# Kernel tuning notes

Measured on AMD Instinct MI355X. Metric: run time of the kernel, lower is better.

Reference implementation:

```python
import jax, jax.numpy as jnp
import numpy as np

B, N, D = 4, 4096, 512
E, H, TOPK = 4, 2048, 1
V_MAX, FEAT_CLAMP = 3.0, 10.0


def setup_inputs() -> dict:
    key = jax.random.key(0)
    ks = jax.random.split(key, 8)
    g = lambda k, shape, s: (jax.random.normal(k, shape, jnp.float32) * s)
    return {
        "x": g(ks[0], (B, N, D), 1.0),
        "gate_w": g(ks[1], (D, E), 0.02), "gate_b": jnp.zeros((E,), jnp.float32),
        "w1": g(ks[2], (E, D, H), 0.02), "b1": jnp.zeros((E, H), jnp.float32),
        "w2": g(ks[3], (E, H, D), 0.02), "b2": jnp.zeros((E, D), jnp.float32),
        "v_w": g(ks[4], (D,), 0.02), "v_b": jnp.zeros((), jnp.float32),
        "out_w": g(ks[5], (2, D), 0.02), "out_b": jnp.zeros((D,), jnp.float32),
        "bk_scale": jnp.asarray(1.0, jnp.float32),
    }


def _moe_ffn(x, gate_w, gate_b, w1, b1, w2, b2):
    # Sparse MoE FFN (eval mode, no dropout): top-k routing, softmax over top-k logits.
    logits = x @ gate_w + gate_b                       # (B,N,E)
    vals, idx = jax.lax.top_k(logits, TOPK)            # (B,N,K)
    wts = jax.nn.softmax(vals, axis=-1)                # (B,N,K); == 1.0 for top_k=1
    wfull = jnp.sum(jax.nn.one_hot(idx, E, dtype=x.dtype) * wts[..., None], axis=-2)  # (B,N,E)
    h = jax.nn.gelu(jnp.einsum('bnd,edh->benh', x, w1) + b1[None, :, None, :])
    y = jnp.einsum('benh,ehd->bend', h, w2) + b2[None, :, None, :]
    return jnp.einsum('bne,bend->bnd', wfull, y)


def _tridiag_green_diag(diag, sup, sub, z):
    # Diagonal of G = (T - z I)^{-1} for tridiagonal T via stable continuant ratios:
    #   L_i = theta_i/theta_{i-1},  R_i = phi_i/phi_{i+1},  G_ii = 1/(L_i + R_i - d_i)
    d = diag.astype(jnp.complex64) - z                 # (B,N)
    s = (sub * sup).astype(jnp.complex64)              # (B,N-1)
    dT = jnp.swapaxes(d, 0, 1)                         # (N,B)
    sT = jnp.swapaxes(s, 0, 1)                         # (N-1,B)

    def step(carry, inp):
        di, si = inp
        nxt = di - si / carry
        return nxt, nxt

    _, Lrest = jax.lax.scan(step, dT[0], (dT[1:], sT))
    L = jnp.concatenate([dT[:1], Lrest], axis=0)       # (N,B)
    _, Rrest = jax.lax.scan(step, dT[-1], (dT[:-1][::-1], sT[::-1]))
    R = jnp.concatenate([dT[-1:], Rrest], axis=0)[::-1]
    G = 1.0 / (L + R - dT)                             # (N,B)
    return jnp.swapaxes(G, 0, 1)                       # (B,N)


def reference(x, gate_w, gate_b, w1, b1, w2, b2, v_w, v_b, out_w, out_b, bk_scale):
    ffn_out = _moe_ffn(x, gate_w, gate_b, w1, b1, w2, b2)        # (B,N,D)
    v = jnp.clip(ffn_out @ v_w + v_b, -V_MAX, V_MAX)             # (B,N)
    he_diag = v - 2.0                                            # h0_diag_base = -2
    ones_off = jnp.ones((x.shape[0], x.shape[1] - 1), x.dtype)   # h0 sub/super = 1
    G = _tridiag_green_diag(he_diag, ones_off, ones_off, jnp.complex64(1j))
    feats = jnp.clip(jnp.stack([G.real, G.imag], axis=-1), -FEAT_CLAMP, FEAT_CLAMP)  # (B,N,2)
    spec = feats @ out_w + out_b                                 # (B,N,D)
    return ffn_out + bk_scale * spec
```

## Files before the change

### kernel.cpp

```cpp
#include <hip/hip_runtime.h>
#include <hip/hip_bf16.h>
#include <stdint.h>

#define TOK 16384
#define NSEQ 4096
#define BATCH 4
#define Dm 512
#define Em 4
#define Hm 2048

typedef __attribute__((ext_vector_type(4))) float f32x4;
typedef __attribute__((ext_vector_type(4))) unsigned int u32x4;

__device__ __forceinline__ unsigned short f2bf(float f) {
    union { float f; uint32_t u; } v; v.f = f;
    uint32_t u = v.u;
    uint32_t r = (u + 0x7FFFu + ((u >> 16) & 1u)) >> 16;
    return (unsigned short)r;
}

struct cpx { float re, im; };
__device__ __forceinline__ cpx cmul(cpx a, cpx b) { return { a.re*b.re - a.im*b.im, a.re*b.im + a.im*b.re }; }
__device__ __forceinline__ cpx csub(cpx a, cpx b) { return { a.re - b.re, a.im - b.im }; }
__device__ __forceinline__ cpx cadd(cpx a, cpx b) { return { a.re + b.re, a.im + b.im }; }
__device__ __forceinline__ cpx cdiv(cpx a, cpx b) {
    float inv = 1.0f / (b.re*b.re + b.im*b.im);
    return { (a.re*b.re + a.im*b.im)*inv, (a.im*b.re - a.re*b.im)*inv };
}

__device__ __forceinline__ void mfma_bf16(f32x4& acc, u32x4 a, u32x4 b) {
    asm("v_mfma_f32_16x16x32_bf16 %0, %1, %2, %0" : "+v"(acc) : "v"(a), "v"(b));
}

#define GLOAD_LDS16(g, l) \
    __builtin_amdgcn_global_load_lds((const __attribute__((address_space(1))) unsigned int*)(g), \
                                     (__attribute__((address_space(3))) unsigned int*)(l), 16, 0, 0)

__global__ __launch_bounds__(256) void gate_kernel(
    const float* __restrict__ x, const float* __restrict__ gate_w, const float* __restrict__ gate_b,
    unsigned short* __restrict__ xbf, int* __restrict__ expert_id)
{
    int wid = threadIdx.x >> 6, lane = threadIdx.x & 63;
    int t0 = (blockIdx.x * 4 + wid) * 8;

    const float4* gw4 = (const float4*)gate_w;
    float4 g[8];
#pragma unroll
    for (int j = 0; j < 8; j++) g[j] = gw4[lane * 8 + j];
    double gb0 = (double)gate_b[0], gb1 = (double)gate_b[1];
    double gb2 = (double)gate_b[2], gb3 = (double)gate_b[3];

    for (int tt = 0; tt < 8; tt++) {
        int t = t0 + tt;
        const float4* x4 = (const float4*)(x + (size_t)t * Dm);
        float4 xa = x4[lane * 2], xb = x4[lane * 2 + 1];

        uint4 pk;
        pk.x = (uint32_t)f2bf(xa.x) | ((uint32_t)f2bf(xa.y) << 16);
        pk.y = (uint32_t)f2bf(xa.z) | ((uint32_t)f2bf(xa.w) << 16);
        pk.z = (uint32_t)f2bf(xb.x) | ((uint32_t)f2bf(xb.y) << 16);
        pk.w = (uint32_t)f2bf(xb.z) | ((uint32_t)f2bf(xb.w) << 16);
        *(uint4*)(xbf + (size_t)t * Dm + lane * 8) = pk;

        float xv[8] = { xa.x, xa.y, xa.z, xa.w, xb.x, xb.y, xb.z, xb.w };
        double s0 = 0, s1 = 0, s2 = 0, s3 = 0;
#pragma unroll
        for (int j = 0; j < 8; j++) {
            s0 += (double)xv[j] * (double)g[j].x;
            s1 += (double)xv[j] * (double)g[j].y;
            s2 += (double)xv[j] * (double)g[j].z;
            s3 += (double)xv[j] * (double)g[j].w;
        }
#pragma unroll
        for (int off = 1; off < 64; off <<= 1) {
            s0 += __shfl_xor(s0, off);
            s1 += __shfl_xor(s1, off);
            s2 += __shfl_xor(s2, off);
            s3 += __shfl_xor(s3, off);
        }
        if (lane == 0) {
            double l0 = s0 + gb0, l1 = s1 + gb1, l2 = s2 + gb2, l3 = s3 + gb3;
            int e = 0; double best = l0;
            if (l1 > best) { best = l1; e = 1; }
            if (l2 > best) { best = l2; e = 2; }
            if (l3 > best) { best = l3; e = 3; }
            expert_id[t] = e;
        }
    }
}

__global__ __launch_bounds__(256) void transpose_cvt(
    const float* __restrict__ w1, const float* __restrict__ w2,
    unsigned short* __restrict__ w1t, unsigned short* __restrict__ w2t)
{
    int z = blockIdx.z;
    const float* src; unsigned short* dst; int R, C;
    if (z < 4) { src = w1 + (size_t)z * Dm * Hm; dst = w1t + (size_t)z * Hm * Dm; R = Dm; C = Hm; }
    else       { src = w2 + (size_t)(z - 4) * Hm * Dm; dst = w2t + (size_t)(z - 4) * Dm * Hm; R = Hm; C = Dm; }
    int c0 = blockIdx.x * 32, r0 = blockIdx.y * 32;
    if (c0 >= C || r0 >= R) return;
    __shared__ float tile[32][33];
    int tx = threadIdx.x & 31, ty = threadIdx.x >> 5;
#pragma unroll
    for (int i = 0; i < 4; i++)
        tile[ty + i * 8][tx] = src[(size_t)(r0 + ty + i * 8) * C + c0 + tx];
    __syncthreads();
#pragma unroll
    for (int i = 0; i < 4; i++)
        dst[(size_t)(c0 + ty + i * 8) * R + r0 + tx] = f2bf(tile[tx][ty + i * 8]);
}

__global__ __launch_bounds__(1024) void route_kernel(
    const int* __restrict__ expert_id, int* __restrict__ counts,
    int* __restrict__ offsets, int* __restrict__ rowmap)
{
    __shared__ int wcnt[16][4];
    __shared__ int woff[16][4];
    int wid = threadIdx.x >> 6, lane = threadIdx.x & 63;
    int base = wid * 1024;

    int myeid[16], myrank[16];
    int run0 = 0, run1 = 0, run2 = 0, run3 = 0;
#pragma unroll
    for (int s = 0; s < 16; s++) {
        int e = expert_id[base + s * 64 + lane];
        myeid[s] = e;
        unsigned long long b0 = __ballot(e & 1);
        unsigned long long b1 = __ballot(e & 2);
        unsigned long long m0 = (e & 1) ? b0 : ~b0;
        unsigned long long m1 = (e & 2) ? b1 : ~b1;
        unsigned long long same = m0 & m1;
        unsigned long long below = same & ((1ull << lane) - 1ull);
        int runh = (e == 0) ? run0 : (e == 1) ? run1 : (e == 2) ? run2 : run3;
        myrank[s] = runh + (int)__popcll(below);
        run0 += (int)__popcll(~b0 & ~b1);
        run1 += (int)__popcll(b0 & ~b1);
        run2 += (int)__popcll(~b0 & b1);
        run3 += (int)__popcll(b0 & b1);
    }
    if (lane == 0) {
        wcnt[wid][0] = run0; wcnt[wid][1] = run1; wcnt[wid][2] = run2; wcnt[wid][3] = run3;
    }
    __syncthreads();
    if (threadIdx.x == 0) {
        int t0 = 0, t1 = 0, t2 = 0, t3 = 0;
        for (int w = 0; w < 16; w++) {
            woff[w][0] = t0; woff[w][1] = t1; woff[w][2] = t2; woff[w][3] = t3;
            t0 += wcnt[w][0]; t1 += wcnt[w][1]; t2 += wcnt[w][2]; t3 += wcnt[w][3];
        }
        counts[0] = t0; counts[1] = t1; counts[2] = t2; counts[3] = t3;
        int o0 = 0, o1 = t0, o2 = t0 + t1, o3 = t0 + t1 + t2;
        offsets[0] = o0; offsets[1] = o1; offsets[2] = o2; offsets[3] = o3;
        for (int w = 0; w < 16; w++) {
            woff[w][0] += o0; woff[w][1] += o1; woff[w][2] += o2; woff[w][3] += o3;
        }
    }
    __syncthreads();
#pragma unroll
    for (int s = 0; s < 16; s++) {
        int e = myeid[s];
        rowmap[woff[wid][e] + myrank[s]] = base + s * 64 + lane;
    }
}

template<int KTOT, int NTOT, bool GATHER_A, bool GELU_EPI>
__global__ __launch_bounds__(256) void gemm_kernel(
    const unsigned short* __restrict__ A, const unsigned short* __restrict__ B,
    const float* __restrict__ bias,
    const int* __restrict__ counts, const int* __restrict__ offsets,
    const int* __restrict__ rowmap,
    unsigned short* __restrict__ Hout, float* __restrict__ Cout,
    const float* __restrict__ v_w, float* __restrict__ vpart)
{
    constexpr int NT = KTOT / 32;
    int e = blockIdx.z;
    int Me = counts[e];
    int mblk = blockIdx.x;
    if (mblk * 128 >= Me) return;
    int base = offsets[e];
    int nblk = blockIdx.y;
    int t = threadIdx.x, wid = t >> 6, lane = t & 63;

    __shared__ __align__(16) unsigned short As[3][128 * 32];
    __shared__ __align__(16) unsigned short Bs[3][128 * 32];

    const unsigned short* agp[2];
    const unsigned short* bgp[2];
#pragma unroll
    for (int c = 0; c < 2; c++) {
        int r = (c * 4 + wid) * 16 + (lane >> 2);
        int g = (lane & 3) ^ ((r >> 1) & 3);
        int mr = mblk * 128 + r; if (mr >= Me) mr = Me - 1;
        int arow = GATHER_A ? rowmap[base + mr] : (base + mr);
        agp[c] = A + (size_t)arow * KTOT + g * 8;
        int nr = nblk * 128 + r;
        bgp[c] = B + ((size_t)e * NTOT + nr) * (size_t)KTOT + g * 8;
    }

    int wm = wid >> 1, wn = wid & 1;
    int g = lane >> 4;
    int r0a = wm * 64 + (lane & 15);
    int r0b = wn * 64 + (lane & 15);
    int abase = r0a * 64 + ((g ^ ((r0a >> 1) & 3)) << 4);
    int bbase = r0b * 64 + ((g ^ ((r0b >> 1) & 3)) << 4);

    f32x4 acc[4][4] = {};

#define STAGE_T(bufi, kt) do { \
    _Pragma("unroll") \
    for (int c = 0; c < 2; c++) { \
        GLOAD_LDS16(agp[c] + (kt) * 32, &As[bufi][(c * 4 + wid) * 512]); \
        GLOAD_LDS16(bgp[c] + (kt) * 32, &Bs[bufi][(c * 4 + wid) * 512]); \
    } \
} while (0)

    STAGE_T(0, 0);
    STAGE_T(1, 1);
    int cur = 0;
    for (int kt = 0; kt < NT; ++kt) {
        int nb = cur + 2; if (nb >= 3) nb -= 3;
        if (kt + 2 < NT) {
            STAGE_T(nb, kt + 2);
            asm volatile("s_waitcnt vmcnt(8)" ::: "memory");
        } else if (kt + 1 < NT) {
            asm volatile("s_waitcnt vmcnt(4)" ::: "memory");
        } else {
            asm volatile("s_waitcnt vmcnt(0)" ::: "memory");
        }
        __builtin_amdgcn_s_barrier();

        const char* ab = (const char*)&As[cur][0];
        const char* bb = (const char*)&Bs[cur][0];
        u32x4 av[4], bv[4];
#pragma unroll
        for (int m = 0; m < 4; m++) av[m] = *(const u32x4*)(ab + abase + m * 1024);
#pragma unroll
        for (int n = 0; n < 4; n++) bv[n] = *(const u32x4*)(bb + bbase + n * 1024);
        __builtin_amdgcn_s_setprio(1);
#pragma unroll
        for (int m = 0; m < 4; m++)
#pragma unroll
            for (int n = 0; n < 4; n++)
                mfma_bf16(acc[m][n], av[m], bv[n]);
        __builtin_amdgcn_s_setprio(0);
        asm volatile("s_waitcnt lgkmcnt(0)" ::: "memory");
        __builtin_amdgcn_s_barrier();
        cur = (cur + 1 == 3) ? 0 : cur + 1;
    }
#undef STAGE_T

    float bb4[4], vw4[4];
#pragma unroll
    for (int n = 0; n < 4; n++) {
        int col = nblk * 128 + wn * 64 + n * 16 + (lane & 15);
        bb4[n] = bias[e * NTOT + col];
        if (!GELU_EPI) vw4[n] = v_w[col];
    }
#pragma unroll
    for (int m = 0; m < 4; m++) {
        int rbase = wm * 64 + m * 16 + ((lane >> 4) << 2);
#pragma unroll
        for (int j = 0; j < 4; j++) {
            int row = mblk * 128 + rbase + j;
            bool ok = row < Me;
            float p = 0.0f;
            int tok = 0;
            if (!GELU_EPI) tok = rowmap[base + (ok ? row : 0)];
#pragma unroll
            for (int n = 0; n < 4; n++) {
                int col = nblk * 128 + wn * 64 + n * 16 + (lane & 15);
                float v = acc[m][n][j] + bb4[n];
                if (GELU_EPI) {
                    if (ok) {
                        float u = 0.7978845608f * (v + 0.044715f * v * v * v);
                        float ex = __expf(2.0f * u);
                        float th = 1.0f - 2.0f / (ex + 1.0f);
                        float hv = 0.5f * v * (1.0f + th);
                        Hout[(size_t)(base + row) * NTOT + col] = f2bf(hv);
                    }
                } else {
                    if (ok) Cout[(size_t)tok * Dm + col] = v;
                    p += v * vw4[n];
                }
            }
            if (!GELU_EPI) {
                p += __shfl_xor(p, 1); p += __shfl_xor(p, 2);
                p += __shfl_xor(p, 4); p += __shfl_xor(p, 8);
                if (ok && (lane & 15) == 0) vpart[tok * 4 + nblk] = p;
            }
        }
    }
}

__global__ __launch_bounds__(256) void vdot2_kernel(
    const float4* __restrict__ vpart, const float* __restrict__ v_b, float* __restrict__ dre)
{
    int t = blockIdx.x * 256 + threadIdx.x;
    float4 p = vpart[t];
    float v = p.x + p.y + p.z + p.w + v_b[0];
    v = fminf(fmaxf(v, -3.0f), 3.0f);
    dre[t] = v - 2.0f;
}

#define SDI(i) ((i) + ((i) >> 6))
__global__ __launch_bounds__(64) void scan_kernel(
    const float* __restrict__ dre, float2* __restrict__ Lf, float2* __restrict__ Rb)
{
    int b = blockIdx.x >> 1, dir = blockIdx.x & 1;
    int lane = threadIdx.x;
    __shared__ float sd[4096 + 64];
    const float* src = dre + b * NSEQ;
    for (int i = lane; i < NSEQ; i += 64)
        sd[SDI(i)] = src[dir ? (NSEQ - 1 - i) : i];
    __syncthreads();

    cpx m00 = {1, 0}, m01 = {0, 0}, m10 = {0, 0}, m11 = {1, 0};
    int s0i = lane * 64;
#pragma unroll 4
    for (int j = 0; j < 64; j++) {
        cpx d = { sd[SDI(s0i + j)], -1.0f };
        cpx n00 = csub(cmul(d, m00), m10);
        cpx n01 = csub(cmul(d, m01), m11);
        m10 = m00; m11 = m01; m00 = n00; m01 = n01;
        if ((j & 15) == 15) {
            float mx = fmaxf(fmaxf(fmaxf(fabsf(m00.re), fabsf(m00.im)), fmaxf(fabsf(m01.re), fabsf(m01.im))),
                             fmaxf(fmaxf(fabsf(m10.re), fabsf(m10.im)), fmaxf(fabsf(m11.re), fabsf(m11.im))));
            float r = 1.0f / mx;
            m00.re *= r; m00.im *= r; m01.re *= r; m01.im *= r;
            m10.re *= r; m10.im *= r; m11.re *= r; m11.im *= r;
        }
    }

#pragma unroll
    for (int off = 1; off < 64; off <<= 1) {
        cpx q00, q01, q10, q11;
        q00.re = __shfl_up(m00.re, off); q00.im = __shfl_up(m00.im, off);
        q01.re = __shfl_up(m01.re, off); q01.im = __shfl_up(m01.im, off);
        q10.re = __shfl_up(m10.re, off); q10.im = __shfl_up(m10.im, off);
        q11.re = __shfl_up(m11.re, off); q11.im = __shfl_up(m11.im, off);
        if (lane >= off) {
            cpx r00 = cadd(cmul(m00, q00), cmul(m01, q10));
            cpx r01 = cadd(cmul(m00, q01), cmul(m01, q11));
            cpx r10 = cadd(cmul(m10, q00), cmul(m11, q10));
            cpx r11 = cadd(cmul(m10, q01), cmul(m11, q11));
            m00 = r00; m01 = r01; m10 = r10; m11 = r11;
            float mx = fmaxf(fmaxf(fmaxf(fabsf(m00.re), fabsf(m00.im)), fmaxf(fabsf(m01.re), fabsf(m01.im))),
                             fmaxf(fmaxf(fabsf(m10.re), fabsf(m10.im)), fmaxf(fabsf(m11.re), fabsf(m11.im))));
            float r = 1.0f / mx;
            m00.re *= r; m00.im *= r; m01.re *= r; m01.im *= r;
            m10.re *= r; m10.im *= r; m11.re *= r; m11.im *= r;
        }
    }

    cpx e00, e10;
    e00.re = __shfl_up(m00.re, 1); e00.im = __shfl_up(m00.im, 1);
    e10.re = __shfl_up(m10.re, 1); e10.im = __shfl_up(m10.im, 1);
    if (lane == 0) { e00 = {1, 0}; e10 = {0, 0}; }

    float2* outp = dir ? Rb : Lf;
    cpx Linv = cdiv(e10, e00);
#pragma unroll 4
    for (int j = 0; j < 64; j++) {
        int p = s0i + j;
        cpx d = { sd[SDI(p)], -1.0f };
        cpx L = csub(d, Linv);
        int idx = dir ? (NSEQ - 1 - p) : p;
        outp[b * NSEQ + idx] = make_float2(L.re, L.im);
        float inv = 1.0f / (L.re * L.re + L.im * L.im);
        Linv.re = L.re * inv; Linv.im = -L.im * inv;
    }
}

__global__ __launch_bounds__(256) void final_kernel(
    float* __restrict__ out, const float* __restrict__ dre,
    const float2* __restrict__ Lf, const float2* __restrict__ Rb,
    const float* __restrict__ out_w, const float* __restrict__ out_b,
    const float* __restrict__ bk)
{
    int t = blockIdx.x * 2 + (threadIdx.x >> 7);
    int c = threadIdx.x & 127;
    float2 L = Lf[t], R = Rb[t];
    float dr = dre[t];
    float denr = L.x + R.x - dr;
    float deni = L.y + R.y + 1.0f;
    float inv = 1.0f / (denr * denr + deni * deni);
    float f0 = fminf(fmaxf(denr * inv, -10.0f), 10.0f);
    float f1 = fminf(fmaxf(-deni * inv, -10.0f), 10.0f);
    float bks = bk[0];
    const float4* ow0 = (const float4*)out_w;
    const float4* ow1 = (const float4*)(out_w + Dm);
    const float4* ob4 = (const float4*)out_b;
    float4* o4 = (float4*)(out + (size_t)t * Dm);
    float4 w0 = ow0[c], w1v = ow1[c], ob = ob4[c];
    float4 y = o4[c];
    y.x += bks * (f0 * w0.x + f1 * w1v.x + ob.x);
    y.y += bks * (f0 * w0.y + f1 * w1v.y + ob.y);
    y.z += bks * (f0 * w0.z + f1 * w1v.z + ob.z);
    y.w += bks * (f0 * w0.w + f1 * w1v.w + ob.w);
    o4[c] = y;
}

constexpr size_t OFF_XBF    = 0;
constexpr size_t OFF_W1T    = 16777216;
constexpr size_t OFF_W2T    = OFF_W1T + 8388608;
constexpr size_t OFF_H      = OFF_W2T + 8388608;
constexpr size_t OFF_ROWMAP = OFF_H + 67108864;
constexpr size_t OFF_EID    = OFF_ROWMAP + 65536;
constexpr size_t OFF_DRE    = OFF_EID + 65536;
constexpr size_t OFF_LF     = OFF_DRE + 65536;
constexpr size_t OFF_RB     = OFF_LF + 131072;
constexpr size_t OFF_CNT    = OFF_RB + 131072;
constexpr size_t OFF_VPART  = OFF_CNT + 64;

extern "C" void kernel_launch(void* const* d_in, const int* in_sizes, int n_in,
                              void* d_out, int out_size, void* d_ws, size_t ws_size,
                              hipStream_t stream)
{
    const float* x      = (const float*)d_in[0];
    const float* gate_w = (const float*)d_in[1];
    const float* gate_b = (const float*)d_in[2];
    const float* w1     = (const float*)d_in[3];
    const float* b1     = (const float*)d_in[4];
    const float* w2     = (const float*)d_in[5];
    const float* b2     = (const float*)d_in[6];
    const float* v_w    = (const float*)d_in[7];
    const float* v_b    = (const float*)d_in[8];
    const float* out_w  = (const float*)d_in[9];
    const float* out_b  = (const float*)d_in[10];
    const float* bk     = (const float*)d_in[11];
    float* out = (float*)d_out;
    char* ws = (char*)d_ws;

    unsigned short* xbf = (unsigned short*)(ws + OFF_XBF);
    unsigned short* w1t = (unsigned short*)(ws + OFF_W1T);
    unsigned short* w2t = (unsigned short*)(ws + OFF_W2T);
    unsigned short* hbf = (unsigned short*)(ws + OFF_H);
    int* rowmap  = (int*)(ws + OFF_ROWMAP);
    int* eid     = (int*)(ws + OFF_EID);
    float* dre   = (float*)(ws + OFF_DRE);
    float2* Lf   = (float2*)(ws + OFF_LF);
    float2* Rb   = (float2*)(ws + OFF_RB);
    int* counts  = (int*)(ws + OFF_CNT);
    int* offsets = counts + 4;
    float* vpart = (float*)(ws + OFF_VPART);

    (void)in_sizes; (void)n_in; (void)out_size; (void)ws_size;

    gate_kernel<<<TOK / 32, 256, 0, stream>>>(x, gate_w, gate_b, xbf, eid);
    transpose_cvt<<<dim3(64, 64, 8), 256, 0, stream>>>(w1, w2, w1t, w2t);
    route_kernel<<<1, 1024, 0, stream>>>(eid, counts, offsets, rowmap);

    gemm_kernel<512, 2048, true, true><<<dim3(128, 16, 4), 256, 0, stream>>>(
        xbf, w1t, b1, counts, offsets, rowmap, hbf, nullptr, nullptr, nullptr);
    gemm_kernel<2048, 512, false, false><<<dim3(128, 4, 4), 256, 0, stream>>>(
        hbf, w2t, b2, counts, offsets, rowmap, nullptr, out, v_w, vpart);

    vdot2_kernel<<<TOK / 256, 256, 0, stream>>>((const float4*)vpart, v_b, dre);
    scan_kernel<<<8, 64, 0, stream>>>(dre, Lf, Rb);
    final_kernel<<<TOK / 2, 256, 0, stream>>>(out, dre, Lf, Rb, out_w, out_b, bk);
}
```

Measured before the change: 198.9 us.

## Merge prep kernels, narrow GEMM2 N-tile, and reorder GEMM1 block grid

Merges the gate/bf16-cast kernel and the weight transpose kernel into one launch using a flat block index. The second GEMM now uses a 64-wide N tile, doubling its block count for better CU occupancy, and vpart/vdot2 are widened to 8 partials per token to match. GEMM1 swaps its grid so that N-blocks vary fastest, which keeps A tiles reused across neighbouring blocks. It also adds launch_bounds minimum occupancy of 4, which could cause register pressure or spills.

```diff
diff --git a/kernel.cpp b/kernel.cpp
--- a/kernel.cpp
+++ b/kernel.cpp
@@ -36,69 +36,80 @@
     __builtin_amdgcn_global_load_lds((const __attribute__((address_space(1))) unsigned int*)(g), \
                                      (__attribute__((address_space(3))) unsigned int*)(l), 16, 0, 0)
 
-__global__ __launch_bounds__(256) void gate_kernel(
+#define GATE_BLOCKS 512
+#define W1T_BLOCKS 4096
+#define W2T_BLOCKS 4096
+__global__ __launch_bounds__(256) void prep_kernel(
     const float* __restrict__ x, const float* __restrict__ gate_w, const float* __restrict__ gate_b,
-    unsigned short* __restrict__ xbf, int* __restrict__ expert_id)
-{
-    int wid = threadIdx.x >> 6, lane = threadIdx.x & 63;
-    int t0 = (blockIdx.x * 4 + wid) * 8;
-
-    const float4* gw4 = (const float4*)gate_w;
-    float4 g[8];
-#pragma unroll
-    for (int j = 0; j < 8; j++) g[j] = gw4[lane * 8 + j];
-    double gb0 = (double)gate_b[0], gb1 = (double)gate_b[1];
-    double gb2 = (double)gate_b[2], gb3 = (double)gate_b[3];
-
-    for (int tt = 0; tt < 8; tt++) {
-        int t = t0 + tt;
-        const float4* x4 = (const float4*)(x + (size_t)t * Dm);
-        float4 xa = x4[lane * 2], xb = x4[lane * 2 + 1];
-
-        uint4 pk;
-        pk.x = (uint32_t)f2bf(xa.x) | ((uint32_t)f2bf(xa.y) << 16);
-        pk.y = (uint32_t)f2bf(xa.z) | ((uint32_t)f2bf(xa.w) << 16);
-        pk.z = (uint32_t)f2bf(xb.x) | ((uint32_t)f2bf(xb.y) << 16);
-        pk.w = (uint32_t)f2bf(xb.z) | ((uint32_t)f2bf(xb.w) << 16);
-        *(uint4*)(xbf + (size_t)t * Dm + lane * 8) = pk;
-
-        float xv[8] = { xa.x, xa.y, xa.z, xa.w, xb.x, xb.y, xb.z, xb.w };
-        double s0 = 0, s1 = 0, s2 = 0, s3 = 0;
-#pragma unroll
-        for (int j = 0; j < 8; j++) {
-            s0 += (double)xv[j] * (double)g[j].x;
-            s1 += (double)xv[j] * (double)g[j].y;
-            s2 += (double)xv[j] * (double)g[j].z;
-            s3 += (double)xv[j] * (double)g[j].w;
-        }
-#pragma unroll
-        for (int off = 1; off < 64; off <<= 1) {
-            s0 += __shfl_xor(s0, off);
-            s1 += __shfl_xor(s1, off);
-            s2 += __shfl_xor(s2, off);
-            s3 += __shfl_xor(s3, off);
-        }
-        if (lane == 0) {
-            double l0 = s0 + gb0, l1 = s1 + gb1, l2 = s2 + gb2, l3 = s3 + gb3;
-            int e = 0; double best = l0;
-            if (l1 > best) { best = l1; e = 1; }
-            if (l2 > best) { best = l2; e = 2; }
-            if (l3 > best) { best = l3; e = 3; }
-            expert_id[t] = e;
-        }
-    }
-}
-
-__global__ __launch_bounds__(256) void transpose_cvt(
     const float* __restrict__ w1, const float* __restrict__ w2,
+    unsigned short* __restrict__ xbf, int* __restrict__ expert_id,
     unsigned short* __restrict__ w1t, unsigned short* __restrict__ w2t)
 {
-    int z = blockIdx.z;
-    const float* src; unsigned short* dst; int R, C;
-    if (z < 4) { src = w1 + (size_t)z * Dm * Hm; dst = w1t + (size_t)z * Hm * Dm; R = Dm; C = Hm; }
-    else       { src = w2 + (size_t)(z - 4) * Hm * Dm; dst = w2t + (size_t)(z - 4) * Dm * Hm; R = Hm; C = Dm; }
-    int c0 = blockIdx.x * 32, r0 = blockIdx.y * 32;
-    if (c0 >= C || r0 >= R) return;
+    int bid = blockIdx.x;
+    if (bid < GATE_BLOCKS) {
+        int wid = threadIdx.x >> 6, lane = threadIdx.x & 63;
+        int t0 = (bid * 4 + wid) * 8;
+        const float4* gw4 = (const float4*)gate_w;
+        float4 g[8];
+#pragma unroll
+        for (int j = 0; j < 8; j++) g[j] = gw4[lane * 8 + j];
+        double gb0 = (double)gate_b[0], gb1 = (double)gate_b[1];
+        double gb2 = (double)gate_b[2], gb3 = (double)gate_b[3];
+
+        for (int tt = 0; tt < 8; tt++) {
+            int t = t0 + tt;
+            const float4* x4 = (const float4*)(x + (size_t)t * Dm);
+            float4 xa = x4[lane * 2], xb = x4[lane * 2 + 1];
+
+            uint4 pk;
+            pk.x = (uint32_t)f2bf(xa.x) | ((uint32_t)f2bf(xa.y) << 16);
+            pk.y = (uint32_t)f2bf(xa.z) | ((uint32_t)f2bf(xa.w) << 16);
+            pk.z = (uint32_t)f2bf(xb.x) | ((uint32_t)f2bf(xb.y) << 16);
+            pk.w = (uint32_t)f2bf(xb.z) | ((uint32_t)f2bf(xb.w) << 16);
+            *(uint4*)(xbf + (size_t)t * Dm + lane * 8) = pk;
+
+            float xv[8] = { xa.x, xa.y, xa.z, xa.w, xb.x, xb.y, xb.z, xb.w };
+            double s0 = 0, s1 = 0, s2 = 0, s3 = 0;
+#pragma unroll
+            for (int j = 0; j < 8; j++) {
+                s0 += (double)xv[j] * (double)g[j].x;
+                s1 += (double)xv[j] * (double)g[j].y;
+                s2 += (double)xv[j] * (double)g[j].z;
+                s3 += (double)xv[j] * (double)g[j].w;
+            }
+#pragma unroll
+            for (int off = 1; off < 64; off <<= 1) {
+                s0 += __shfl_xor(s0, off);
+                s1 += __shfl_xor(s1, off);
+                s2 += __shfl_xor(s2, off);
+                s3 += __shfl_xor(s3, off);
+            }
+            if (lane == 0) {
+                double l0 = s0 + gb0, l1 = s1 + gb1, l2 = s2 + gb2, l3 = s3 + gb3;
+                int e = 0; double best = l0;
+                if (l1 > best) { best = l1; e = 1; }
+                if (l2 > best) { best = l2; e = 2; }
+                if (l3 > best) { best = l3; e = 3; }
+                expert_id[t] = e;
+            }
+        }
+        return;
+    }
+
+    const float* src; unsigned short* dst; int R, C, c0, r0;
+    if (bid < GATE_BLOCKS + W1T_BLOCKS) {
+        int idx = bid - GATE_BLOCKS;
+        int e = idx >> 10, rem = idx & 1023;
+        src = w1 + (size_t)e * Dm * Hm; dst = w1t + (size_t)e * Hm * Dm;
+        R = Dm; C = Hm;
+        c0 = (rem >> 4) * 32; r0 = (rem & 15) * 32;
+    } else {
+        int idx = bid - GATE_BLOCKS - W1T_BLOCKS;
+        int e = idx >> 10, rem = idx & 1023;
+        src = w2 + (size_t)e * Hm * Dm; dst = w2t + (size_t)e * Dm * Hm;
+        R = Hm; C = Dm;
+        c0 = (rem >> 6) * 32; r0 = (rem & 63) * 32;
+    }
     __shared__ float tile[32][33];
     int tx = threadIdx.x & 31, ty = threadIdx.x >> 5;
 #pragma unroll
@@ -163,8 +174,8 @@
     }
 }
 
-template<int KTOT, int NTOT, bool GATHER_A, bool GELU_EPI>
-__global__ __launch_bounds__(256) void gemm_kernel(
+template<int KTOT, int NTOT, int BN, bool MSWAP, bool GATHER_A, bool GELU_EPI>
+__global__ __launch_bounds__(256, 4) void gemm_kernel(
     const unsigned short* __restrict__ A, const unsigned short* __restrict__ B,
     const float* __restrict__ bias,
     const int* __restrict__ counts, const int* __restrict__ offsets,
@@ -173,45 +184,54 @@
     const float* __restrict__ v_w, float* __restrict__ vpart)
 {
     constexpr int NT = KTOT / 32;
+    constexpr int NREP = BN / 32;
+    constexpr int BLOADS = BN / 64;
     int e = blockIdx.z;
     int Me = counts[e];
-    int mblk = blockIdx.x;
+    int mblk = MSWAP ? blockIdx.x : blockIdx.y;
     if (mblk * 128 >= Me) return;
     int base = offsets[e];
-    int nblk = blockIdx.y;
+    int nblk = MSWAP ? blockIdx.y : blockIdx.x;
     int t = threadIdx.x, wid = t >> 6, lane = t & 63;
 
     __shared__ __align__(16) unsigned short As[3][128 * 32];
-    __shared__ __align__(16) unsigned short Bs[3][128 * 32];
+    __shared__ __align__(16) unsigned short Bs[3][BN * 32];
 
     const unsigned short* agp[2];
-    const unsigned short* bgp[2];
 #pragma unroll
     for (int c = 0; c < 2; c++) {
-        int r = (c * 4 + wid) * 16 + (lane >> 2);
-        int g = (lane & 3) ^ ((r >> 1) & 3);
+        int f = c * 256 + t;
+        int r = f >> 2;
+        int g = (f & 3) ^ ((r >> 1) & 3);
         int mr = mblk * 128 + r; if (mr >= Me) mr = Me - 1;
         int arow = GATHER_A ? rowmap[base + mr] : (base + mr);
         agp[c] = A + (size_t)arow * KTOT + g * 8;
-        int nr = nblk * 128 + r;
+    }
+    const unsigned short* bgp[BLOADS];
+#pragma unroll
+    for (int c = 0; c < BLOADS; c++) {
+        int f = c * 256 + t;
+        int r = f >> 2;
+        int g = (f & 3) ^ ((r >> 1) & 3);
+        int nr = nblk * BN + r;
         bgp[c] = B + ((size_t)e * NTOT + nr) * (size_t)KTOT + g * 8;
     }
 
     int wm = wid >> 1, wn = wid & 1;
     int g = lane >> 4;
     int r0a = wm * 64 + (lane & 15);
-    int r0b = wn * 64 + (lane & 15);
+    int r0b = wn * (BN / 2) + (lane & 15);
     int abase = r0a * 64 + ((g ^ ((r0a >> 1) & 3)) << 4);
     int bbase = r0b * 64 + ((g ^ ((r0b >> 1) & 3)) << 4);
 
-    f32x4 acc[4][4] = {};
+    f32x4 acc[4][NREP] = {};
 
 #define STAGE_T(bufi, kt) do { \
+    GLOAD_LDS16(agp[0] + (kt) * 32, &As[bufi][(size_t)(0 * 4 + wid) * 512]); \
+    GLOAD_LDS16(agp[1] + (kt) * 32, &As[bufi][(size_t)(1 * 4 + wid) * 512]); \
     _Pragma("unroll") \
-    for (int c = 0; c < 2; c++) { \
-        GLOAD_LDS16(agp[c] + (kt) * 32, &As[bufi][(c * 4 + wid) * 512]); \
-        GLOAD_LDS16(bgp[c] + (kt) * 32, &Bs[bufi][(c * 4 + wid) * 512]); \
-    } \
+    for (int c = 0; c < BLOADS; c++) \
+        GLOAD_LDS16(bgp[c] + (kt) * 32, &Bs[bufi][(size_t)(c * 4 + wid) * 512]); \
 } while (0)
 
     STAGE_T(0, 0);
@@ -221,9 +241,11 @@
         int nb = cur + 2; if (nb >= 3) nb -= 3;
         if (kt + 2 < NT) {
             STAGE_T(nb, kt + 2);
-            asm volatile("s_waitcnt vmcnt(8)" ::: "memory");
+            if constexpr (BN == 128) asm volatile("s_waitcnt vmcnt(8)" ::: "memory");
+            else                     asm volatile("s_waitcnt vmcnt(6)" ::: "memory");
         } else if (kt + 1 < NT) {
-            asm volatile("s_waitcnt vmcnt(4)" ::: "memory");
+            if constexpr (BN == 128) asm volatile("s_waitcnt vmcnt(4)" ::: "memory");
+            else                     asm volatile("s_waitcnt vmcnt(3)" ::: "memory");
         } else {
             asm volatile("s_waitcnt vmcnt(0)" ::: "memory");
         }
@@ -231,16 +253,16 @@
 
         const char* ab = (const char*)&As[cur][0];
         const char* bb = (const char*)&Bs[cur][0];
-        u32x4 av[4], bv[4];
+        u32x4 av[4], bv[NREP];
 #pragma unroll
         for (int m = 0; m < 4; m++) av[m] = *(const u32x4*)(ab + abase + m * 1024);
 #pragma unroll
-        for (int n = 0; n < 4; n++) bv[n] = *(const u32x4*)(bb + bbase + n * 1024);
+        for (int n = 0; n < NREP; n++) bv[n] = *(const u32x4*)(bb + bbase + n * 1024);
         __builtin_amdgcn_s_setprio(1);
 #pragma unroll
         for (int m = 0; m < 4; m++)
 #pragma unroll
-            for (int n = 0; n < 4; n++)
+            for (int n = 0; n < NREP; n++)
                 mfma_bf16(acc[m][n], av[m], bv[n]);
         __builtin_amdgcn_s_setprio(0);
         asm volatile("s_waitcnt lgkmcnt(0)" ::: "memory");
@@ -249,10 +271,10 @@
     }
 #undef STAGE_T
 
-    float bb4[4], vw4[4];
-#pragma unroll
-    for (int n = 0; n < 4; n++) {
-        int col = nblk * 128 + wn * 64 + n * 16 + (lane & 15);
+    float bb4[NREP], vw4[NREP];
+#pragma unroll
+    for (int n = 0; n < NREP; n++) {
+        int col = nblk * BN + wn * (BN / 2) + n * 16 + (lane & 15);
         bb4[n] = bias[e * NTOT + col];
         if (!GELU_EPI) vw4[n] = v_w[col];
     }
@@ -267,8 +289,8 @@
             int tok = 0;
             if (!GELU_EPI) tok = rowmap[base + (ok ? row : 0)];
 #pragma unroll
-            for (int n = 0; n < 4; n++) {
-                int col = nblk * 128 + wn * 64 + n * 16 + (lane & 15);
+            for (int n = 0; n < NREP; n++) {
+                int col = nblk * BN + wn * (BN / 2) + n * 16 + (lane & 15);
                 float v = acc[m][n][j] + bb4[n];
                 if (GELU_EPI) {
                     if (ok) {
@@ -286,7 +308,7 @@
             if (!GELU_EPI) {
                 p += __shfl_xor(p, 1); p += __shfl_xor(p, 2);
                 p += __shfl_xor(p, 4); p += __shfl_xor(p, 8);
-                if (ok && (lane & 15) == 0) vpart[tok * 4 + nblk] = p;
+                if (ok && (lane & 15) == 0) vpart[(size_t)tok * (NTOT / BN) + nblk] = p;
             }
         }
     }
@@ -296,8 +318,8 @@
     const float4* __restrict__ vpart, const float* __restrict__ v_b, float* __restrict__ dre)
 {
     int t = blockIdx.x * 256 + threadIdx.x;
-    float4 p = vpart[t];
-    float v = p.x + p.y + p.z + p.w + v_b[0];
+    float4 a = vpart[t * 2], b = vpart[t * 2 + 1];
+    float v = a.x + a.y + a.z + a.w + b.x + b.y + b.z + b.w + v_b[0];
     v = fminf(fmaxf(v, -3.0f), 3.0f);
     dre[t] = v - 2.0f;
 }
@@ -446,13 +468,13 @@
 
     (void)in_sizes; (void)n_in; (void)out_size; (void)ws_size;
 
-    gate_kernel<<<TOK / 32, 256, 0, stream>>>(x, gate_w, gate_b, xbf, eid);
-    transpose_cvt<<<dim3(64, 64, 8), 256, 0, stream>>>(w1, w2, w1t, w2t);
+    prep_kernel<<<GATE_BLOCKS + W1T_BLOCKS + W2T_BLOCKS, 256, 0, stream>>>(
+        x, gate_w, gate_b, w1, w2, xbf, eid, w1t, w2t);
     route_kernel<<<1, 1024, 0, stream>>>(eid, counts, offsets, rowmap);
 
-    gemm_kernel<512, 2048, true, true><<<dim3(128, 16, 4), 256, 0, stream>>>(
+    gemm_kernel<512, 2048, 128, false, true, true><<<dim3(16, 128, 4), 256, 0, stream>>>(
         xbf, w1t, b1, counts, offsets, rowmap, hbf, nullptr, nullptr, nullptr);
-    gemm_kernel<2048, 512, false, false><<<dim3(128, 4, 4), 256, 0, stream>>>(
+    gemm_kernel<2048, 512, 64, true, false, false><<<dim3(128, 8, 4), 256, 0, stream>>>(
         hbf, w2t, b2, counts, offsets, rowmap, nullptr, out, v_w, vpart);
 
     vdot2_kernel<<<TOK / 256, 256, 0, stream>>>((const float4*)vpart, v_b, dre);
```

After: 213.0 us. 1.07x slower.
